# Optimization experiments

Hardware: AMD Instinct MI355X
Metric: run time of the kernel (lower is better)

The kernel has to match this reference:

```python
import jax, jax.numpy as jnp
import numpy as np
import math

HEADS = 4
DK = 64            # dim // heads
TEMP = 1.0
LMAX = 2048        # max segment length (for padded ragged attention)


def setup_inputs() -> dict:
    key = jax.random.key(0)
    ks = jax.random.split(key, 6)
    T, H, B = 1024, 256, 16
    # ragged lengths alternating 2048/1024 -> N = 24576
    lengths = np.tile(np.array([2048, 1024], dtype=np.int64), B // 2)
    N = int(lengths.sum())
    s = 1.0 / math.sqrt(H)
    return {
        "go_mat": jax.random.normal(ks[0], (T, H), jnp.float32),
        "node_h": jax.random.normal(ks[1], (N, H), jnp.float32),
        "Wq": jax.random.normal(ks[2], (H, H), jnp.float32) * s,
        "Wk": jax.random.normal(ks[3], (H, H), jnp.float32) * s,
        "Wv": jax.random.normal(ks[4], (H, H), jnp.float32) * s,
        "Wproj": jax.random.normal(ks[5], (H, H), jnp.float32) * s,
        "num_nodes_per_graph": jnp.asarray(lengths),
    }


def reference(go_mat, node_h, Wq, Wk, Wv, Wproj, num_nodes_per_graph):
    lengths = num_nodes_per_graph
    B = lengths.shape[0]
    N, H = node_h.shape
    T = go_mat.shape[0]

    # segment bookkeeping: graph id and within-graph offset for each node
    cum = jnp.cumsum(lengths)                       # [B]
    starts = cum - lengths                          # [B]
    g = jnp.searchsorted(cum, jnp.arange(N), side="right")  # [N] graph id
    off = jnp.arange(N) - starts[g]                 # [N] position within graph

    # projections (torch Linear: x @ W.T)
    Q = (go_mat @ Wq.T).reshape(T, HEADS, DK).transpose(1, 0, 2)   # [h,T,dk]
    K = node_h @ Wk.T                                              # [N,H]
    V = node_h @ Wv.T

    # scatter packed nodes into padded [B, Lmax, H]
    Kp = jnp.zeros((B, LMAX, H), K.dtype).at[g, off].set(K)
    Vp = jnp.zeros((B, LMAX, H), V.dtype).at[g, off].set(V)
    Kp = Kp.reshape(B, LMAX, HEADS, DK).transpose(0, 2, 1, 3)      # [B,h,L,dk]
    Vp = Vp.reshape(B, LMAX, HEADS, DK).transpose(0, 2, 1, 3)

    scores = jnp.einsum("htd,bhld->bhtl", Q, Kp) / (math.sqrt(DK) * TEMP)
    valid = jnp.arange(LMAX)[None, :] < lengths[:, None]           # [B,L]
    scores = jnp.where(valid[:, None, None, :], scores, jnp.float32(-1e30))
    attn = jax.nn.softmax(scores, axis=-1)                         # [B,h,T,L]

    ctx = jnp.einsum("bhtl,bhld->bhtd", attn, Vp)                  # [B,h,T,dk]
    ctx = ctx.transpose(0, 2, 1, 3).reshape(B, T, H)               # [B,T,H]
    return ctx @ Wproj.T
```

## Files before the change

### kernel.cpp

```cpp
#include <hip/hip_runtime.h>
#include <math.h>

#define HEADS 4
#define DK 64
#define HD 256

typedef __attribute__((ext_vector_type(8))) __bf16 bf16x8;
typedef __attribute__((ext_vector_type(4))) float floatx4;

union BF8 { ushort u[8]; bf16x8 v; };

__device__ __forceinline__ ushort f2bf(float f) {
  union { float f; unsigned u; } x; x.f = f;
  return (ushort)((x.u + 0x7FFF + ((x.u >> 16) & 1)) >> 16);
}
__device__ __forceinline__ ushort f2bf_fast(float f) {
  union { float f; unsigned u; } x; x.f = f;
  return (ushort)((x.u + 0x8000u) >> 16);
}

#define GLDS(g, l) __builtin_amdgcn_global_load_lds(                      \
    (const __attribute__((address_space(1))) unsigned*)(g),               \
    (__attribute__((address_space(3))) unsigned*)(l), 16, 0, 0)

__global__ __launch_bounds__(256) void cvt_swz(const float* __restrict__ x,
                                               ushort* __restrict__ y, int rows) {
  const int idx = blockIdx.x * 256 + threadIdx.x;
  const int row = idx >> 5, gr = idx & 31;
  if (row >= rows) return;
  const int chunk = gr >> 3, g = gr & 7;
  const float* src = x + (size_t)row * 256 + gr * 8;
  float4 a = *(const float4*)src;
  float4 bq = *(const float4*)(src + 4);
  const int phys = g ^ (row & 7);
  ushort* dst = y + (size_t)row * 256 + chunk * 64 + phys * 8;
  ushort4 o0 = {f2bf(a.x), f2bf(a.y), f2bf(a.z), f2bf(a.w)};
  ushort4 o1 = {f2bf(bq.x), f2bf(bq.y), f2bf(bq.z), f2bf(bq.w)};
  *(ushort4*)dst = o0;
  *(ushort4*)(dst + 4) = o1;
}

__global__ __launch_bounds__(256) void cvt_swz_w(const float* __restrict__ w0,
                                                 const float* __restrict__ w1,
                                                 const float* __restrict__ w2,
                                                 const float* __restrict__ w3,
                                                 ushort* __restrict__ y) {
  const float* srcs[4] = {w0, w1, w2, w3};
  const float* x = srcs[blockIdx.y];
  ushort* yo = y + (size_t)blockIdx.y * HD * HD;
  const int idx = blockIdx.x * 256 + threadIdx.x;
  const int row = idx >> 5, gr = idx & 31;
  const int chunk = gr >> 3, g = gr & 7;
  const float* src = x + (size_t)row * 256 + gr * 8;
  float4 a = *(const float4*)src;
  float4 bq = *(const float4*)(src + 4);
  const int phys = g ^ (row & 7);
  ushort* dst = yo + (size_t)row * 256 + chunk * 64 + phys * 8;
  ushort4 o0 = {f2bf(a.x), f2bf(a.y), f2bf(a.z), f2bf(a.w)};
  ushort4 o1 = {f2bf(bq.x), f2bf(bq.y), f2bf(bq.z), f2bf(bq.w)};
  *(ushort4*)dst = o0;
  *(ushort4*)(dst + 4) = o1;
}

template <int MODE>
__global__ __launch_bounds__(256) void gemm_bf16(const ushort* __restrict__ A,
                                                 const ushort* __restrict__ W,
                                                 ushort* __restrict__ C, int M,
                                                 int ldc) {
  __shared__ ushort As[128 * 64];
  __shared__ ushort Ws[64 * 64];
  const int tid = threadIdx.x, lane = tid & 63, w = tid >> 6;
  const int quad = lane >> 4, l15 = lane & 15;
  const int m0 = blockIdx.x * 128, n0 = blockIdx.y * 64;
  const int wm = w & 1, wn = w >> 1;

  floatx4 acc[4][2];
#pragma unroll
  for (int mt = 0; mt < 4; ++mt)
#pragma unroll
    for (int nt = 0; nt < 2; ++nt) acc[mt][nt] = (floatx4){0.f, 0.f, 0.f, 0.f};

  for (int k0 = 0; k0 < 256; k0 += 64) {
    __syncthreads();
#pragma unroll
    for (int t = 0; t < 4; ++t)
      GLDS(A + (size_t)(m0 + w * 32 + t * 8 + (lane >> 3)) * 256 + k0 + (lane & 7) * 8,
           &As[(w * 32 + t * 8) * 64]);
#pragma unroll
    for (int t = 0; t < 2; ++t)
      GLDS(W + (size_t)(n0 + w * 16 + t * 8 + (lane >> 3)) * 256 + k0 + (lane & 7) * 8,
           &Ws[(w * 16 + t * 8) * 64]);
    __syncthreads();

    bf16x8 af[4][2], bfr[2][2];
#pragma unroll
    for (int kk = 0; kk < 2; ++kk) {
      const int pg = ((kk * 4 + quad) ^ (l15 & 7)) * 8;
#pragma unroll
      for (int mt = 0; mt < 4; ++mt)
        af[mt][kk] = *(const bf16x8*)&As[(wm * 64 + mt * 16 + l15) * 64 + pg];
#pragma unroll
      for (int nt = 0; nt < 2; ++nt)
        bfr[nt][kk] = *(const bf16x8*)&Ws[(wn * 32 + nt * 16 + l15) * 64 + pg];
    }
#pragma unroll
    for (int kk = 0; kk < 2; ++kk)
#pragma unroll
      for (int mt = 0; mt < 4; ++mt)
#pragma unroll
        for (int nt = 0; nt < 2; ++nt)
          acc[mt][nt] = __builtin_amdgcn_mfma_f32_16x16x32_bf16(
              af[mt][kk], bfr[nt][kk], acc[mt][nt], 0, 0, 0);
  }

#pragma unroll
  for (int mt = 0; mt < 4; ++mt)
#pragma unroll
    for (int nt = 0; nt < 2; ++nt) {
      const int col = n0 + wn * 32 + nt * 16 + l15;
      if (MODE == 2) {
        const int d = col & 63;
        const int g = mt * 2 + (quad >> 1);
        const int node = m0 + wm * 64 + (g ^ (d & 7)) * 8 + (quad & 1) * 4;
        ushort4 o = {f2bf(acc[mt][nt][0]), f2bf(acc[mt][nt][1]),
                     f2bf(acc[mt][nt][2]), f2bf(acc[mt][nt][3])};
        *(ushort4*)&C[(size_t)col * ldc + node] = o;
      } else {
#pragma unroll
        for (int r = 0; r < 4; ++r) {
          const int row = m0 + wm * 64 + mt * 16 + quad * 4 + r;
          if (MODE == 3) {
            ((float*)C)[(size_t)row * 256 + col] = acc[mt][nt][r];
          } else {
            int cc = col;
            if (MODE == 1)
              cc = (col & ~63) | (((((col >> 3) & 7) ^ (row & 7))) << 3) | (col & 7);
            C[(size_t)row * 256 + cc] = f2bf(acc[mt][nt][r]);
          }
        }
      }
    }
}

__global__ __launch_bounds__(512, 4) void attn_mfma(
    const ushort* __restrict__ Qb, const ushort* __restrict__ Kg,
    const ushort* __restrict__ Vt, const int* __restrict__ lens,
    ushort* __restrict__ ctxb, int T, int N) {
  __shared__ ushort Ks[2][64 * 64];
  __shared__ ushort Vs[2][64 * 64];
  __shared__ ushort Ps[8 * 16 * 72];

  const int tid = threadIdx.x, lane = tid & 63, wave = tid >> 6;
  const int quad = lane >> 4, l15 = lane & 15;
  const int h = blockIdx.y, b = blockIdx.z;
  int start = 0;
  for (int i = 0; i < b; ++i) start += lens[i];
  const int len = lens[b];

  const int srow = wave * 8 + (lane >> 3);
  const int scol = (lane & 7) * 8;

  const int tq = blockIdx.x * 128 + wave * 16 + l15;
  bf16x8 qa[2];
#pragma unroll
  for (int kk = 0; kk < 2; ++kk)
    qa[kk] = *(const bf16x8*)(Qb + (size_t)tq * 256 + h * 64 + kk * 32 + quad * 8);

  BF8 onesu;
#pragma unroll
  for (int j = 0; j < 8; ++j) onesu.u[j] = 0x3F80;
  const bf16x8 ones = onesu.v;

  floatx4 o[4], lacc = (floatx4){0.f, 0.f, 0.f, 0.f};
#pragma unroll
  for (int n = 0; n < 4; ++n) o[n] = (floatx4){0.f, 0.f, 0.f, 0.f};

  const float sc = 0.18033688011112042f;
  ushort* pw = &Ps[wave * 16 * 72];

  GLDS(Kg + (size_t)(start + srow) * 256 + h * 64 + scol, &Ks[0][wave * 8 * 64]);
  GLDS(Vt + (size_t)(h * 64 + srow) * (size_t)N + start + scol, &Vs[0][wave * 8 * 64]);

  int buf = 0;
  for (int j0 = 0; j0 < len; j0 += 64, buf ^= 1) {
    __syncthreads();
    const int jn = j0 + 64;
    if (jn < len) {
      GLDS(Kg + (size_t)(start + jn + srow) * 256 + h * 64 + scol,
           &Ks[buf ^ 1][wave * 8 * 64]);
      GLDS(Vt + (size_t)(h * 64 + srow) * (size_t)N + start + jn + scol,
           &Vs[buf ^ 1][wave * 8 * 64]);
    }

    floatx4 st[4];
#pragma unroll
    for (int t = 0; t < 4; ++t) st[t] = (floatx4){0.f, 0.f, 0.f, 0.f};
#pragma unroll
    for (int kk = 0; kk < 2; ++kk) {
#pragma unroll
      for (int t = 0; t < 4; ++t) {
        bf16x8 kf = *(const bf16x8*)&Ks[buf][(t * 16 + l15) * 64 +
                                            ((kk * 4 + quad) ^ (l15 & 7)) * 8];
        st[t] = __builtin_amdgcn_mfma_f32_16x16x32_bf16(qa[kk], kf, st[t], 0, 0, 0);
      }
    }

    const bool full = jn <= len;
#pragma unroll
    for (int t = 0; t < 4; ++t) {
      const bool v = full || (j0 + t * 16 + l15 < len);
#pragma unroll
      for (int r = 0; r < 4; ++r) {
        const float u = v ? fmaf(st[t][r], sc, -32.0f) : -1e30f;
        pw[(quad * 4 + r) * 72 + t * 16 + l15] = f2bf_fast(exp2f(u));
      }
    }

#pragma unroll
    for (int ks = 0; ks < 2; ++ks) {
      bf16x8 pa = *(const bf16x8*)&pw[l15 * 72 + ks * 32 + quad * 8];
      lacc = __builtin_amdgcn_mfma_f32_16x16x32_bf16(pa, ones, lacc, 0, 0, 0);
#pragma unroll
      for (int n = 0; n < 4; ++n) {
        bf16x8 vf = *(const bf16x8*)&Vs[buf][(n * 16 + l15) * 64 +
                                            ((ks * 4 + quad) ^ (l15 & 7)) * 8];
        o[n] = __builtin_amdgcn_mfma_f32_16x16x32_bf16(pa, vf, o[n], 0, 0, 0);
      }
    }
  }

  float inv[4];
#pragma unroll
  for (int r = 0; r < 4; ++r) inv[r] = 1.0f / lacc[r];
  const int q0 = blockIdx.x * 128 + wave * 16 + quad * 4;
  ushort* cb = ctxb + ((size_t)b * T + q0) * 256;
#pragma unroll
  for (int n = 0; n < 4; ++n)
#pragma unroll
    for (int r = 0; r < 4; ++r) {
      const int colg = n * 2 + (l15 >> 3);
      const int cc = h * 64 + ((colg ^ ((q0 + r) & 7)) << 3) | (l15 & 7);
      cb[(size_t)r * 256 + cc] = f2bf(o[n][r] * inv[r]);
    }
}

extern "C" void kernel_launch(void* const* d_in, const int* in_sizes, int n_in,
                              void* d_out, int out_size, void* d_ws, size_t ws_size,
                              hipStream_t stream) {
  const float* go     = (const float*)d_in[0];
  const float* node_h = (const float*)d_in[1];
  const float* Wq     = (const float*)d_in[2];
  const float* Wk     = (const float*)d_in[3];
  const float* Wv     = (const float*)d_in[4];
  const float* Wproj  = (const float*)d_in[5];
  const int*   lens   = (const int*)d_in[6];

  const int T = in_sizes[0] / HD;
  const int N = in_sizes[1] / HD;
  const int B = in_sizes[6];

  char* p = (char*)d_ws;
  ushort* ctxb = (ushort*)p;            p += (size_t)B * T * HD * 2;
  ushort* nodebf = (ushort*)p;          p += (size_t)N * HD * 2;
  ushort* Kgb = (ushort*)p;             p += (size_t)N * HD * 2;
  ushort* Vtb = (ushort*)p;             p += (size_t)N * HD * 2;
  ushort* gobf = (ushort*)p;            p += (size_t)T * HD * 2;
  ushort* Qbf = (ushort*)p;             p += (size_t)T * HD * 2;
  ushort* wbf = (ushort*)p;             p += (size_t)4 * HD * HD * 2;
  ushort* wqbf = wbf;
  ushort* wkbf = wbf + (size_t)HD * HD;
  ushort* wvbf = wbf + (size_t)2 * HD * HD;
  ushort* wpbf = wbf + (size_t)3 * HD * HD;

  cvt_swz<<<(T * 32 + 255) / 256, 256, 0, stream>>>(go, gobf, T);
  cvt_swz<<<(N * 32 + 255) / 256, 256, 0, stream>>>(node_h, nodebf, N);
  cvt_swz_w<<<dim3(32, 4), 256, 0, stream>>>(Wq, Wk, Wv, Wproj, wbf);

  gemm_bf16<0><<<dim3(T / 128, 4), 256, 0, stream>>>(gobf, wqbf, Qbf, T, 0);
  gemm_bf16<1><<<dim3(N / 128, 4), 256, 0, stream>>>(nodebf, wkbf, Kgb, N, 0);
  gemm_bf16<2><<<dim3(N / 128, 4), 256, 0, stream>>>(nodebf, wvbf, Vtb, N, N);

  attn_mfma<<<dim3(T / 128, HEADS, B), 512, 0, stream>>>(Qbf, Kgb, Vtb, lens, ctxb, T, N);

  gemm_bf16<3><<<dim3((B * T) / 128, 4), 256, 0, stream>>>(ctxb, wpbf, (ushort*)d_out, B * T, 0);
}
```

Measured before the change: 185.8 us.

## Give each attention wave two query tiles and merge K/V projection kernels

The attention kernel drops to 256 threads per block, with each wave handling 32 queries (two 16-row tiles). Each K and V fragment read from LDS is therefore reused across two MFMAs, which halves LDS fragment traffic per FLOP. The row-sum is now accumulated in registers from the fp32 probabilities instead of through an MFMA against a ones vector, and scores are computed transposed so the P tile can be written as packed ushort4 stores. Separately, the K and V projections are merged into one launch, and V's transpose is staged through LDS for coalesced 16-byte stores. The costs are higher register pressure and fewer waves per block to hide latency.

```diff
diff --git a/kernel.cpp b/kernel.cpp
--- a/kernel.cpp
+++ b/kernel.cpp
@@ -7,8 +7,6 @@
 
 typedef __attribute__((ext_vector_type(8))) __bf16 bf16x8;
 typedef __attribute__((ext_vector_type(4))) float floatx4;
-
-union BF8 { ushort u[8]; bf16x8 v; };
 
 __device__ __forceinline__ ushort f2bf(float f) {
   union { float f; unsigned u; } x; x.f = f;
@@ -62,93 +60,125 @@
   *(ushort4*)(dst + 4) = o1;
 }
 
+#define GEMM_BODY(APTR, WPTR)                                                  \
+  floatx4 acc[4][2];                                                           \
+  _Pragma("unroll") for (int mt = 0; mt < 4; ++mt)                             \
+      _Pragma("unroll") for (int nt = 0; nt < 2; ++nt)                         \
+          acc[mt][nt] = (floatx4){0.f, 0.f, 0.f, 0.f};                         \
+  for (int k0 = 0; k0 < 256; k0 += 64) {                                       \
+    __syncthreads();                                                           \
+    _Pragma("unroll") for (int t = 0; t < 4; ++t)                              \
+        GLDS(APTR + (size_t)(m0 + w * 32 + t * 8 + (lane >> 3)) * 256 + k0 +   \
+                 (lane & 7) * 8,                                               \
+             &As[(w * 32 + t * 8) * 64]);                                      \
+    _Pragma("unroll") for (int t = 0; t < 2; ++t)                              \
+        GLDS(WPTR + (size_t)(n0 + w * 16 + t * 8 + (lane >> 3)) * 256 + k0 +   \
+                 (lane & 7) * 8,                                               \
+             &Ws[(w * 16 + t * 8) * 64]);                                      \
+    __syncthreads();                                                           \
+    bf16x8 af[4][2], bfr[2][2];                                                \
+    _Pragma("unroll") for (int kk = 0; kk < 2; ++kk) {                         \
+      const int pg = ((kk * 4 + quad) ^ (l15 & 7)) * 8;                        \
+      _Pragma("unroll") for (int mt = 0; mt < 4; ++mt)                         \
+          af[mt][kk] = *(const bf16x8*)&As[(wm * 64 + mt * 16 + l15) * 64 + pg]; \
+      _Pragma("unroll") for (int nt = 0; nt < 2; ++nt)                         \
+          bfr[nt][kk] = *(const bf16x8*)&Ws[(wn * 32 + nt * 16 + l15) * 64 + pg]; \
+    }                                                                          \
+    _Pragma("unroll") for (int kk = 0; kk < 2; ++kk)                           \
+        _Pragma("unroll") for (int mt = 0; mt < 4; ++mt)                       \
+            _Pragma("unroll") for (int nt = 0; nt < 2; ++nt)                   \
+                acc[mt][nt] = __builtin_amdgcn_mfma_f32_16x16x32_bf16(         \
+                    af[mt][kk], bfr[nt][kk], acc[mt][nt], 0, 0, 0);            \
+  }
+
 template <int MODE>
 __global__ __launch_bounds__(256) void gemm_bf16(const ushort* __restrict__ A,
                                                  const ushort* __restrict__ W,
-                                                 ushort* __restrict__ C, int M,
-                                                 int ldc) {
+                                                 ushort* __restrict__ C, int M) {
   __shared__ ushort As[128 * 64];
   __shared__ ushort Ws[64 * 64];
   const int tid = threadIdx.x, lane = tid & 63, w = tid >> 6;
   const int quad = lane >> 4, l15 = lane & 15;
   const int m0 = blockIdx.x * 128, n0 = blockIdx.y * 64;
   const int wm = w & 1, wn = w >> 1;
-
-  floatx4 acc[4][2];
-#pragma unroll
-  for (int mt = 0; mt < 4; ++mt)
-#pragma unroll
-    for (int nt = 0; nt < 2; ++nt) acc[mt][nt] = (floatx4){0.f, 0.f, 0.f, 0.f};
-
-  for (int k0 = 0; k0 < 256; k0 += 64) {
-    __syncthreads();
-#pragma unroll
-    for (int t = 0; t < 4; ++t)
-      GLDS(A + (size_t)(m0 + w * 32 + t * 8 + (lane >> 3)) * 256 + k0 + (lane & 7) * 8,
-           &As[(w * 32 + t * 8) * 64]);
-#pragma unroll
-    for (int t = 0; t < 2; ++t)
-      GLDS(W + (size_t)(n0 + w * 16 + t * 8 + (lane >> 3)) * 256 + k0 + (lane & 7) * 8,
-           &Ws[(w * 16 + t * 8) * 64]);
-    __syncthreads();
-
-    bf16x8 af[4][2], bfr[2][2];
-#pragma unroll
-    for (int kk = 0; kk < 2; ++kk) {
-      const int pg = ((kk * 4 + quad) ^ (l15 & 7)) * 8;
-#pragma unroll
-      for (int mt = 0; mt < 4; ++mt)
-        af[mt][kk] = *(const bf16x8*)&As[(wm * 64 + mt * 16 + l15) * 64 + pg];
-#pragma unroll
-      for (int nt = 0; nt < 2; ++nt)
-        bfr[nt][kk] = *(const bf16x8*)&Ws[(wn * 32 + nt * 16 + l15) * 64 + pg];
-    }
-#pragma unroll
-    for (int kk = 0; kk < 2; ++kk)
-#pragma unroll
-      for (int mt = 0; mt < 4; ++mt)
-#pragma unroll
-        for (int nt = 0; nt < 2; ++nt)
-          acc[mt][nt] = __builtin_amdgcn_mfma_f32_16x16x32_bf16(
-              af[mt][kk], bfr[nt][kk], acc[mt][nt], 0, 0, 0);
-  }
-
+  GEMM_BODY(A, W)
 #pragma unroll
   for (int mt = 0; mt < 4; ++mt)
 #pragma unroll
     for (int nt = 0; nt < 2; ++nt) {
       const int col = n0 + wn * 32 + nt * 16 + l15;
-      if (MODE == 2) {
-        const int d = col & 63;
-        const int g = mt * 2 + (quad >> 1);
-        const int node = m0 + wm * 64 + (g ^ (d & 7)) * 8 + (quad & 1) * 4;
+#pragma unroll
+      for (int r = 0; r < 4; ++r) {
+        const int row = m0 + wm * 64 + mt * 16 + quad * 4 + r;
+        if (MODE == 3)
+          ((float*)C)[(size_t)row * 256 + col] = acc[mt][nt][r];
+        else
+          C[(size_t)row * 256 + col] = f2bf(acc[mt][nt][r]);
+      }
+    }
+}
+
+__global__ __launch_bounds__(256) void gemm_kv(const ushort* __restrict__ A,
+                                               const ushort* __restrict__ Wk,
+                                               const ushort* __restrict__ Wv,
+                                               ushort* __restrict__ Ck,
+                                               ushort* __restrict__ Cv, int N) {
+  __shared__ ushort As[128 * 64];
+  __shared__ ushort Ws[64 * 64];
+  __shared__ ushort Ts[64 * 136];
+  const int tid = threadIdx.x, lane = tid & 63, w = tid >> 6;
+  const int quad = lane >> 4, l15 = lane & 15;
+  const int m0 = blockIdx.x * 128, n0 = blockIdx.y * 64;
+  const int wm = w & 1, wn = w >> 1;
+  const ushort* W = blockIdx.z ? Wv : Wk;
+  GEMM_BODY(A, W)
+  if (blockIdx.z == 0) {
+#pragma unroll
+    for (int mt = 0; mt < 4; ++mt)
+#pragma unroll
+      for (int nt = 0; nt < 2; ++nt) {
+        const int col = n0 + wn * 32 + nt * 16 + l15;
+#pragma unroll
+        for (int r = 0; r < 4; ++r) {
+          const int row = m0 + wm * 64 + mt * 16 + quad * 4 + r;
+          const int cc =
+              (col & ~63) | (((((col >> 3) & 7) ^ (row & 7))) << 3) | (col & 7);
+          Ck[(size_t)row * 256 + cc] = f2bf(acc[mt][nt][r]);
+        }
+      }
+  } else {
+#pragma unroll
+    for (int mt = 0; mt < 4; ++mt)
+#pragma unroll
+      for (int nt = 0; nt < 2; ++nt) {
+        const int d_rel = wn * 32 + nt * 16 + l15;
+        const int node_rel = wm * 64 + mt * 16 + quad * 4;
         ushort4 o = {f2bf(acc[mt][nt][0]), f2bf(acc[mt][nt][1]),
                      f2bf(acc[mt][nt][2]), f2bf(acc[mt][nt][3])};
-        *(ushort4*)&C[(size_t)col * ldc + node] = o;
-      } else {
-#pragma unroll
-        for (int r = 0; r < 4; ++r) {
-          const int row = m0 + wm * 64 + mt * 16 + quad * 4 + r;
-          if (MODE == 3) {
-            ((float*)C)[(size_t)row * 256 + col] = acc[mt][nt][r];
-          } else {
-            int cc = col;
-            if (MODE == 1)
-              cc = (col & ~63) | (((((col >> 3) & 7) ^ (row & 7))) << 3) | (col & 7);
-            C[(size_t)row * 256 + cc] = f2bf(acc[mt][nt][r]);
-          }
-        }
-      }
-    }
-}
-
-__global__ __launch_bounds__(512, 4) void attn_mfma(
+        *(ushort4*)&Ts[d_rel * 136 + node_rel] = o;
+      }
+    __syncthreads();
+    const int d_rel = tid >> 2;
+    const int cseg = (tid & 3) * 32;
+    const int d = n0 + d_rel;
+#pragma unroll
+    for (int i = 0; i < 4; ++i) {
+      const int col = cseg + i * 8;
+      const int gl = (col >> 3) & 7;
+      const int chunk = col >> 6;
+      uint4 v = *(const uint4*)&Ts[d_rel * 136 + col];
+      *(uint4*)&Cv[(size_t)d * N + m0 + chunk * 64 + ((gl ^ (d & 7)) << 3)] = v;
+    }
+  }
+}
+
+__global__ __launch_bounds__(256, 3) void attn_mfma(
     const ushort* __restrict__ Qb, const ushort* __restrict__ Kg,
     const ushort* __restrict__ Vt, const int* __restrict__ lens,
     ushort* __restrict__ ctxb, int T, int N) {
   __shared__ ushort Ks[2][64 * 64];
   __shared__ ushort Vs[2][64 * 64];
-  __shared__ ushort Ps[8 * 16 * 72];
+  __shared__ ushort Ps[4 * 32 * 72];
 
   const int tid = threadIdx.x, lane = tid & 63, wave = tid >> 6;
   const int quad = lane >> 4, l15 = lane & 15;
@@ -157,91 +187,132 @@
   for (int i = 0; i < b; ++i) start += lens[i];
   const int len = lens[b];
 
-  const int srow = wave * 8 + (lane >> 3);
+  const int q0 = blockIdx.x * 128 + wave * 32;
+  bf16x8 qb[2][2];
+#pragma unroll
+  for (int qt = 0; qt < 2; ++qt)
+#pragma unroll
+    for (int kk = 0; kk < 2; ++kk)
+      qb[qt][kk] = *(const bf16x8*)(Qb + (size_t)(q0 + qt * 16 + l15) * 256 +
+                                    h * 64 + kk * 32 + quad * 8);
+
+  floatx4 o[2][4];
+#pragma unroll
+  for (int qt = 0; qt < 2; ++qt)
+#pragma unroll
+    for (int nt = 0; nt < 4; ++nt) o[qt][nt] = (floatx4){0.f, 0.f, 0.f, 0.f};
+  float lsum[2] = {0.f, 0.f};
+
+  const float sc = 0.18033688011112042f;
+  ushort* pw = &Ps[wave * 32 * 72];
+
+  const int srow = (lane >> 3);
   const int scol = (lane & 7) * 8;
 
-  const int tq = blockIdx.x * 128 + wave * 16 + l15;
-  bf16x8 qa[2];
-#pragma unroll
-  for (int kk = 0; kk < 2; ++kk)
-    qa[kk] = *(const bf16x8*)(Qb + (size_t)tq * 256 + h * 64 + kk * 32 + quad * 8);
-
-  BF8 onesu;
-#pragma unroll
-  for (int j = 0; j < 8; ++j) onesu.u[j] = 0x3F80;
-  const bf16x8 ones = onesu.v;
-
-  floatx4 o[4], lacc = (floatx4){0.f, 0.f, 0.f, 0.f};
-#pragma unroll
-  for (int n = 0; n < 4; ++n) o[n] = (floatx4){0.f, 0.f, 0.f, 0.f};
-
-  const float sc = 0.18033688011112042f;
-  ushort* pw = &Ps[wave * 16 * 72];
-
-  GLDS(Kg + (size_t)(start + srow) * 256 + h * 64 + scol, &Ks[0][wave * 8 * 64]);
-  GLDS(Vt + (size_t)(h * 64 + srow) * (size_t)N + start + scol, &Vs[0][wave * 8 * 64]);
+  GLDS(Kg + (size_t)(start + wave * 8 + srow) * 256 + h * 64 + scol,
+       &Ks[0][(wave * 8) * 64]);
+  GLDS(Kg + (size_t)(start + wave * 8 + 32 + srow) * 256 + h * 64 + scol,
+       &Ks[0][(wave * 8 + 32) * 64]);
+  GLDS(Vt + (size_t)(h * 64 + wave * 8 + srow) * (size_t)N + start + scol,
+       &Vs[0][(wave * 8) * 64]);
+  GLDS(Vt + (size_t)(h * 64 + wave * 8 + 32 + srow) * (size_t)N + start + scol,
+       &Vs[0][(wave * 8 + 32) * 64]);
 
   int buf = 0;
   for (int j0 = 0; j0 < len; j0 += 64, buf ^= 1) {
     __syncthreads();
     const int jn = j0 + 64;
     if (jn < len) {
-      GLDS(Kg + (size_t)(start + jn + srow) * 256 + h * 64 + scol,
-           &Ks[buf ^ 1][wave * 8 * 64]);
-      GLDS(Vt + (size_t)(h * 64 + srow) * (size_t)N + start + jn + scol,
-           &Vs[buf ^ 1][wave * 8 * 64]);
-    }
-
-    floatx4 st[4];
-#pragma unroll
-    for (int t = 0; t < 4; ++t) st[t] = (floatx4){0.f, 0.f, 0.f, 0.f};
+      GLDS(Kg + (size_t)(start + jn + wave * 8 + srow) * 256 + h * 64 + scol,
+           &Ks[buf ^ 1][(wave * 8) * 64]);
+      GLDS(Kg + (size_t)(start + jn + wave * 8 + 32 + srow) * 256 + h * 64 + scol,
+           &Ks[buf ^ 1][(wave * 8 + 32) * 64]);
+      GLDS(Vt + (size_t)(h * 64 + wave * 8 + srow) * (size_t)N + start + jn + scol,
+           &Vs[buf ^ 1][(wave * 8) * 64]);
+      GLDS(Vt + (size_t)(h * 64 + wave * 8 + 32 + srow) * (size_t)N + start + jn + scol,
+           &Vs[buf ^ 1][(wave * 8 + 32) * 64]);
+    }
+
+    floatx4 st[4][2];
+#pragma unroll
+    for (int t = 0; t < 4; ++t)
+#pragma unroll
+      for (int qt = 0; qt < 2; ++qt) st[t][qt] = (floatx4){0.f, 0.f, 0.f, 0.f};
 #pragma unroll
     for (int kk = 0; kk < 2; ++kk) {
 #pragma unroll
       for (int t = 0; t < 4; ++t) {
         bf16x8 kf = *(const bf16x8*)&Ks[buf][(t * 16 + l15) * 64 +
                                             ((kk * 4 + quad) ^ (l15 & 7)) * 8];
-        st[t] = __builtin_amdgcn_mfma_f32_16x16x32_bf16(qa[kk], kf, st[t], 0, 0, 0);
-      }
-    }
-
-    const bool full = jn <= len;
-#pragma unroll
-    for (int t = 0; t < 4; ++t) {
-      const bool v = full || (j0 + t * 16 + l15 < len);
+        st[t][0] = __builtin_amdgcn_mfma_f32_16x16x32_bf16(kf, qb[0][kk], st[t][0], 0, 0, 0);
+        st[t][1] = __builtin_amdgcn_mfma_f32_16x16x32_bf16(kf, qb[1][kk], st[t][1], 0, 0, 0);
+      }
+    }
+
+    if (jn <= len) {
+#pragma unroll
+      for (int t = 0; t < 4; ++t)
+#pragma unroll
+        for (int qt = 0; qt < 2; ++qt) {
+          float p[4];
+#pragma unroll
+          for (int r = 0; r < 4; ++r) p[r] = exp2f(fmaf(st[t][qt][r], sc, -32.0f));
+          lsum[qt] += (p[0] + p[1]) + (p[2] + p[3]);
+          ushort4 pk = {f2bf_fast(p[0]), f2bf_fast(p[1]), f2bf_fast(p[2]),
+                        f2bf_fast(p[3])};
+          *(ushort4*)&pw[(qt * 16 + l15) * 72 + t * 16 + quad * 4] = pk;
+        }
+    } else {
+#pragma unroll
+      for (int t = 0; t < 4; ++t)
+#pragma unroll
+        for (int qt = 0; qt < 2; ++qt) {
+          float p[4];
+#pragma unroll
+          for (int r = 0; r < 4; ++r) {
+            const bool v = (j0 + t * 16 + quad * 4 + r) < len;
+            p[r] = v ? exp2f(fmaf(st[t][qt][r], sc, -32.0f)) : 0.0f;
+          }
+          lsum[qt] += (p[0] + p[1]) + (p[2] + p[3]);
+          ushort4 pk = {f2bf_fast(p[0]), f2bf_fast(p[1]), f2bf_fast(p[2]),
+                        f2bf_fast(p[3])};
+          *(ushort4*)&pw[(qt * 16 + l15) * 72 + t * 16 + quad * 4] = pk;
+        }
+    }
+
+#pragma unroll
+    for (int ks = 0; ks < 2; ++ks) {
+      bf16x8 pa0 = *(const bf16x8*)&pw[l15 * 72 + ks * 32 + quad * 8];
+      bf16x8 pa1 = *(const bf16x8*)&pw[(16 + l15) * 72 + ks * 32 + quad * 8];
+#pragma unroll
+      for (int nt = 0; nt < 4; ++nt) {
+        bf16x8 vf = *(const bf16x8*)&Vs[buf][(nt * 16 + l15) * 64 +
+                                            ((ks * 4 + quad) ^ (l15 & 7)) * 8];
+        o[0][nt] = __builtin_amdgcn_mfma_f32_16x16x32_bf16(pa0, vf, o[0][nt], 0, 0, 0);
+        o[1][nt] = __builtin_amdgcn_mfma_f32_16x16x32_bf16(pa1, vf, o[1][nt], 0, 0, 0);
+      }
+    }
+  }
+
+#pragma unroll
+  for (int qt = 0; qt < 2; ++qt) {
+    float lt = lsum[qt];
+    lt += __shfl_xor(lt, 16);
+    lt += __shfl_xor(lt, 32);
+    float inv[4];
+#pragma unroll
+    for (int r = 0; r < 4; ++r) inv[r] = 1.0f / __shfl(lt, quad * 4 + r);
+    const int qrow0 = q0 + qt * 16 + quad * 4;
+    ushort* cb = ctxb + ((size_t)b * T + qrow0) * 256;
+#pragma unroll
+    for (int nt = 0; nt < 4; ++nt)
 #pragma unroll
       for (int r = 0; r < 4; ++r) {
-        const float u = v ? fmaf(st[t][r], sc, -32.0f) : -1e30f;
-        pw[(quad * 4 + r) * 72 + t * 16 + l15] = f2bf_fast(exp2f(u));
-      }
-    }
-
-#pragma unroll
-    for (int ks = 0; ks < 2; ++ks) {
-      bf16x8 pa = *(const bf16x8*)&pw[l15 * 72 + ks * 32 + quad * 8];
-      lacc = __builtin_amdgcn_mfma_f32_16x16x32_bf16(pa, ones, lacc, 0, 0, 0);
-#pragma unroll
-      for (int n = 0; n < 4; ++n) {
-        bf16x8 vf = *(const bf16x8*)&Vs[buf][(n * 16 + l15) * 64 +
-                                            ((ks * 4 + quad) ^ (l15 & 7)) * 8];
-        o[n] = __builtin_amdgcn_mfma_f32_16x16x32_bf16(pa, vf, o[n], 0, 0, 0);
-      }
-    }
+        const int colg = nt * 2 + (l15 >> 3);
+        const int cc = h * 64 + (((colg ^ ((qrow0 + r) & 7)) << 3) | (l15 & 7));
+        cb[(size_t)r * 256 + cc] = f2bf(o[qt][nt][r] * inv[r]);
+      }
   }
-
-  float inv[4];
-#pragma unroll
-  for (int r = 0; r < 4; ++r) inv[r] = 1.0f / lacc[r];
-  const int q0 = blockIdx.x * 128 + wave * 16 + quad * 4;
-  ushort* cb = ctxb + ((size_t)b * T + q0) * 256;
-#pragma unroll
-  for (int n = 0; n < 4; ++n)
-#pragma unroll
-    for (int r = 0; r < 4; ++r) {
-      const int colg = n * 2 + (l15 >> 3);
-      const int cc = h * 64 + ((colg ^ ((q0 + r) & 7)) << 3) | (l15 & 7);
-      cb[(size_t)r * 256 + cc] = f2bf(o[n][r] * inv[r]);
-    }
 }
 
 extern "C" void kernel_launch(void* const* d_in, const int* in_sizes, int n_in,
@@ -276,11 +347,10 @@
   cvt_swz<<<(N * 32 + 255) / 256, 256, 0, stream>>>(node_h, nodebf, N);
   cvt_swz_w<<<dim3(32, 4), 256, 0, stream>>>(Wq, Wk, Wv, Wproj, wbf);
 
-  gemm_bf16<0><<<dim3(T / 128, 4), 256, 0, stream>>>(gobf, wqbf, Qbf, T, 0);
-  gemm_bf16<1><<<dim3(N / 128, 4), 256, 0, stream>>>(nodebf, wkbf, Kgb, N, 0);
-  gemm_bf16<2><<<dim3(N / 128, 4), 256, 0, stream>>>(nodebf, wvbf, Vtb, N, N);
-
-  attn_mfma<<<dim3(T / 128, HEADS, B), 512, 0, stream>>>(Qbf, Kgb, Vtb, lens, ctxb, T, N);
-
-  gemm_bf16<3><<<dim3((B * T) / 128, 4), 256, 0, stream>>>(ctxb, wpbf, (ushort*)d_out, B * T, 0);
-}
+  gemm_bf16<0><<<dim3(T / 128, 4), 256, 0, stream>>>(gobf, wqbf, Qbf, T);
+  gemm_kv<<<dim3(N / 128, 4, 2), 256, 0, stream>>>(nodebf, wkbf, wvbf, Kgb, Vtb, N);
+
+  attn_mfma<<<dim3(T / 128, HEADS, B), 256, 0, stream>>>(Qbf, Kgb, Vtb, lens, ctxb, T, N);
+
+  gemm_bf16<3><<<dim3((B * T) / 128, 4), 256, 0, stream>>>(ctxb, wpbf, (ushort*)d_out, B * T);
+}
```

New measurement: 194.7 us. +4.8%, slower.

## Split attention over fixed 1024-key chunks and add combine pass

Applied to the files above, without the earlier changes.

Attention now splits each ragged segment into 1024-key chunks, one block per chunk, so long and short graphs give equal-sized work items and the grid is balanced. Each block handles 32 query rows per wave with a transposed score MFMA, sums row totals in registers instead of an extra ones-MFMA, and packs exp values with perm. A new combine kernel adds up the partial outputs and row sums and normalises them. This costs extra fp32 partial traffic through memory and one more launch. The two input conversions are also merged into one launch, and nodebf shares workspace with the partial buffers.

```diff
diff --git a/kernel.cpp b/kernel.cpp
--- a/kernel.cpp
+++ b/kernel.cpp
@@ -8,32 +8,44 @@
 typedef __attribute__((ext_vector_type(8))) __bf16 bf16x8;
 typedef __attribute__((ext_vector_type(4))) float floatx4;
 
-union BF8 { ushort u[8]; bf16x8 v; };
-
 __device__ __forceinline__ ushort f2bf(float f) {
   union { float f; unsigned u; } x; x.f = f;
   return (ushort)((x.u + 0x7FFF + ((x.u >> 16) & 1)) >> 16);
 }
-__device__ __forceinline__ ushort f2bf_fast(float f) {
-  union { float f; unsigned u; } x; x.f = f;
-  return (ushort)((x.u + 0x8000u) >> 16);
+
+#if __has_builtin(__builtin_amdgcn_exp2f)
+#define EXP2(x) __builtin_amdgcn_exp2f(x)
+#else
+#define EXP2(x) exp2f(x)
+#endif
+
+__device__ __forceinline__ unsigned pack_bf2(float lo, float hi) {
+  union { float f; unsigned u; } a, b;
+  a.f = lo; b.f = hi;
+  return __builtin_amdgcn_perm(b.u + 0x8000u, a.u + 0x8000u, 0x07060302u);
 }
 
 #define GLDS(g, l) __builtin_amdgcn_global_load_lds(                      \
     (const __attribute__((address_space(1))) unsigned*)(g),               \
     (__attribute__((address_space(3))) unsigned*)(l), 16, 0, 0)
 
-__global__ __launch_bounds__(256) void cvt_swz(const float* __restrict__ x,
-                                               ushort* __restrict__ y, int rows) {
+__global__ __launch_bounds__(256) void cvt_all(const float* __restrict__ go,
+                                               const float* __restrict__ nh,
+                                               ushort* __restrict__ gobf,
+                                               ushort* __restrict__ nodebf,
+                                               int T, int N) {
   const int idx = blockIdx.x * 256 + threadIdx.x;
   const int row = idx >> 5, gr = idx & 31;
-  if (row >= rows) return;
+  if (row >= T + N) return;
+  const float* x; ushort* y; int r;
+  if (row < T) { x = go; y = gobf; r = row; }
+  else         { x = nh; y = nodebf; r = row - T; }
   const int chunk = gr >> 3, g = gr & 7;
-  const float* src = x + (size_t)row * 256 + gr * 8;
+  const float* src = x + (size_t)r * 256 + gr * 8;
   float4 a = *(const float4*)src;
   float4 bq = *(const float4*)(src + 4);
-  const int phys = g ^ (row & 7);
-  ushort* dst = y + (size_t)row * 256 + chunk * 64 + phys * 8;
+  const int phys = g ^ (r & 7);
+  ushort* dst = y + (size_t)r * 256 + chunk * 64 + phys * 8;
   ushort4 o0 = {f2bf(a.x), f2bf(a.y), f2bf(a.z), f2bf(a.w)};
   ushort4 o1 = {f2bf(bq.x), f2bf(bq.y), f2bf(bq.z), f2bf(bq.w)};
   *(ushort4*)dst = o0;
@@ -67,8 +79,8 @@
                                                  const ushort* __restrict__ W,
                                                  ushort* __restrict__ C, int M,
                                                  int ldc) {
-  __shared__ ushort As[128 * 64];
-  __shared__ ushort Ws[64 * 64];
+  __shared__ __align__(16) ushort As[128 * 64];
+  __shared__ __align__(16) ushort Ws[64 * 64];
   const int tid = threadIdx.x, lane = tid & 63, w = tid >> 6;
   const int quad = lane >> 4, l15 = lane & 15;
   const int m0 = blockIdx.x * 128, n0 = blockIdx.y * 64;
@@ -142,106 +154,192 @@
     }
 }
 
-__global__ __launch_bounds__(512, 4) void attn_mfma(
+__global__ __launch_bounds__(256, 3) void attn_split(
     const ushort* __restrict__ Qb, const ushort* __restrict__ Kg,
     const ushort* __restrict__ Vt, const int* __restrict__ lens,
-    ushort* __restrict__ ctxb, int T, int N) {
-  __shared__ ushort Ks[2][64 * 64];
-  __shared__ ushort Vs[2][64 * 64];
-  __shared__ ushort Ps[8 * 16 * 72];
+    float* __restrict__ Opart, float* __restrict__ Lpart,
+    int T, int N, int Bc) {
+  __shared__ __align__(16) ushort Ks[2][64 * 64];
+  __shared__ __align__(16) ushort Vs[2][64 * 64];
+  __shared__ __align__(16) ushort Ps[4 * 32 * 72];
 
   const int tid = threadIdx.x, lane = tid & 63, wave = tid >> 6;
   const int quad = lane >> 4, l15 = lane & 15;
-  const int h = blockIdx.y, b = blockIdx.z;
-  int start = 0;
-  for (int i = 0; i < b; ++i) start += lens[i];
-  const int len = lens[b];
-
-  const int srow = wave * 8 + (lane >> 3);
+  const int h = blockIdx.y;
+
+  int z = blockIdx.z, b, start = 0, len = 0, off = -1;
+  for (b = 0; b < Bc; ++b) {
+    len = lens[b];
+    const int s = (len + 1023) >> 10;
+    if (z < s) { off = z << 10; break; }
+    z -= s; start += len;
+  }
+  if (off < 0) return;
+  const int kcnt = min(1024, len - off);
+  const int kbeg = start + off;
+
+  const int q0 = blockIdx.x * 128 + wave * 32;
+  bf16x8 qb[2][2];
+#pragma unroll
+  for (int qt = 0; qt < 2; ++qt)
+#pragma unroll
+    for (int kk = 0; kk < 2; ++kk)
+      qb[qt][kk] = *(const bf16x8*)(Qb + (size_t)(q0 + qt * 16 + l15) * 256 +
+                                    h * 64 + kk * 32 + quad * 8);
+
+  floatx4 o[2][4];
+#pragma unroll
+  for (int qt = 0; qt < 2; ++qt)
+#pragma unroll
+    for (int nt = 0; nt < 4; ++nt) o[qt][nt] = (floatx4){0.f, 0.f, 0.f, 0.f};
+  float lsum[2] = {0.f, 0.f};
+
+  const float sc = 0.18033688011112042f;
+  ushort* pw = &Ps[wave * 32 * 72];
+
+  const int srow = lane >> 3;
   const int scol = (lane & 7) * 8;
 
-  const int tq = blockIdx.x * 128 + wave * 16 + l15;
-  bf16x8 qa[2];
-#pragma unroll
-  for (int kk = 0; kk < 2; ++kk)
-    qa[kk] = *(const bf16x8*)(Qb + (size_t)tq * 256 + h * 64 + kk * 32 + quad * 8);
-
-  BF8 onesu;
-#pragma unroll
-  for (int j = 0; j < 8; ++j) onesu.u[j] = 0x3F80;
-  const bf16x8 ones = onesu.v;
-
-  floatx4 o[4], lacc = (floatx4){0.f, 0.f, 0.f, 0.f};
-#pragma unroll
-  for (int n = 0; n < 4; ++n) o[n] = (floatx4){0.f, 0.f, 0.f, 0.f};
-
-  const float sc = 0.18033688011112042f;
-  ushort* pw = &Ps[wave * 16 * 72];
-
-  GLDS(Kg + (size_t)(start + srow) * 256 + h * 64 + scol, &Ks[0][wave * 8 * 64]);
-  GLDS(Vt + (size_t)(h * 64 + srow) * (size_t)N + start + scol, &Vs[0][wave * 8 * 64]);
+  GLDS(Kg + (size_t)(kbeg + wave * 8 + srow) * 256 + h * 64 + scol,
+       &Ks[0][(wave * 8) * 64]);
+  GLDS(Kg + (size_t)(kbeg + wave * 8 + 32 + srow) * 256 + h * 64 + scol,
+       &Ks[0][(wave * 8 + 32) * 64]);
+  GLDS(Vt + (size_t)(h * 64 + wave * 8 + srow) * (size_t)N + kbeg + scol,
+       &Vs[0][(wave * 8) * 64]);
+  GLDS(Vt + (size_t)(h * 64 + wave * 8 + 32 + srow) * (size_t)N + kbeg + scol,
+       &Vs[0][(wave * 8 + 32) * 64]);
 
   int buf = 0;
-  for (int j0 = 0; j0 < len; j0 += 64, buf ^= 1) {
+  for (int j0 = 0; j0 < kcnt; j0 += 64, buf ^= 1) {
     __syncthreads();
     const int jn = j0 + 64;
-    if (jn < len) {
-      GLDS(Kg + (size_t)(start + jn + srow) * 256 + h * 64 + scol,
-           &Ks[buf ^ 1][wave * 8 * 64]);
-      GLDS(Vt + (size_t)(h * 64 + srow) * (size_t)N + start + jn + scol,
-           &Vs[buf ^ 1][wave * 8 * 64]);
-    }
-
-    floatx4 st[4];
-#pragma unroll
-    for (int t = 0; t < 4; ++t) st[t] = (floatx4){0.f, 0.f, 0.f, 0.f};
+    if (jn < kcnt) {
+      GLDS(Kg + (size_t)(kbeg + jn + wave * 8 + srow) * 256 + h * 64 + scol,
+           &Ks[buf ^ 1][(wave * 8) * 64]);
+      GLDS(Kg + (size_t)(kbeg + jn + wave * 8 + 32 + srow) * 256 + h * 64 + scol,
+           &Ks[buf ^ 1][(wave * 8 + 32) * 64]);
+      GLDS(Vt + (size_t)(h * 64 + wave * 8 + srow) * (size_t)N + kbeg + jn + scol,
+           &Vs[buf ^ 1][(wave * 8) * 64]);
+      GLDS(Vt + (size_t)(h * 64 + wave * 8 + 32 + srow) * (size_t)N + kbeg + jn + scol,
+           &Vs[buf ^ 1][(wave * 8 + 32) * 64]);
+    }
+
+    floatx4 st[4][2];
+#pragma unroll
+    for (int t = 0; t < 4; ++t)
+#pragma unroll
+      for (int qt = 0; qt < 2; ++qt) st[t][qt] = (floatx4){0.f, 0.f, 0.f, 0.f};
 #pragma unroll
     for (int kk = 0; kk < 2; ++kk) {
 #pragma unroll
       for (int t = 0; t < 4; ++t) {
         bf16x8 kf = *(const bf16x8*)&Ks[buf][(t * 16 + l15) * 64 +
                                             ((kk * 4 + quad) ^ (l15 & 7)) * 8];
-        st[t] = __builtin_amdgcn_mfma_f32_16x16x32_bf16(qa[kk], kf, st[t], 0, 0, 0);
+        st[t][0] = __builtin_amdgcn_mfma_f32_16x16x32_bf16(kf, qb[0][kk], st[t][0], 0, 0, 0);
+        st[t][1] = __builtin_amdgcn_mfma_f32_16x16x32_bf16(kf, qb[1][kk], st[t][1], 0, 0, 0);
       }
     }
 
-    const bool full = jn <= len;
-#pragma unroll
-    for (int t = 0; t < 4; ++t) {
-      const bool v = full || (j0 + t * 16 + l15 < len);
-#pragma unroll
-      for (int r = 0; r < 4; ++r) {
-        const float u = v ? fmaf(st[t][r], sc, -32.0f) : -1e30f;
-        pw[(quad * 4 + r) * 72 + t * 16 + l15] = f2bf_fast(exp2f(u));
+    if (jn <= kcnt) {
+#pragma unroll
+      for (int t = 0; t < 4; ++t)
+#pragma unroll
+        for (int qt = 0; qt < 2; ++qt) {
+          float p[4];
+#pragma unroll
+          for (int r = 0; r < 4; ++r) p[r] = EXP2(fmaf(st[t][qt][r], sc, -32.0f));
+          lsum[qt] += (p[0] + p[1]) + (p[2] + p[3]);
+          uint2 pk = {pack_bf2(p[0], p[1]), pack_bf2(p[2], p[3])};
+          *(uint2*)&pw[(qt * 16 + l15) * 72 + t * 16 + quad * 4] = pk;
+        }
+    } else {
+#pragma unroll
+      for (int t = 0; t < 4; ++t)
+#pragma unroll
+        for (int qt = 0; qt < 2; ++qt) {
+          float p[4];
+#pragma unroll
+          for (int r = 0; r < 4; ++r) {
+            const bool v = (j0 + t * 16 + quad * 4 + r) < kcnt;
+            p[r] = v ? EXP2(fmaf(st[t][qt][r], sc, -32.0f)) : 0.0f;
+          }
+          lsum[qt] += (p[0] + p[1]) + (p[2] + p[3]);
+          uint2 pk = {pack_bf2(p[0], p[1]), pack_bf2(p[2], p[3])};
+          *(uint2*)&pw[(qt * 16 + l15) * 72 + t * 16 + quad * 4] = pk;
+        }
+    }
+
+#pragma unroll
+    for (int ks = 0; ks < 2; ++ks) {
+      bf16x8 pa0 = *(const bf16x8*)&pw[l15 * 72 + ks * 32 + quad * 8];
+      bf16x8 pa1 = *(const bf16x8*)&pw[(16 + l15) * 72 + ks * 32 + quad * 8];
+#pragma unroll
+      for (int nt = 0; nt < 4; ++nt) {
+        bf16x8 vf = *(const bf16x8*)&Vs[buf][(nt * 16 + l15) * 64 +
+                                            ((ks * 4 + quad) ^ (l15 & 7)) * 8];
+        o[0][nt] = __builtin_amdgcn_mfma_f32_16x16x32_bf16(pa0, vf, o[0][nt], 0, 0, 0);
+        o[1][nt] = __builtin_amdgcn_mfma_f32_16x16x32_bf16(pa1, vf, o[1][nt], 0, 0, 0);
       }
     }
-
-#pragma unroll
-    for (int ks = 0; ks < 2; ++ks) {
-      bf16x8 pa = *(const bf16x8*)&pw[l15 * 72 + ks * 32 + quad * 8];
-      lacc = __builtin_amdgcn_mfma_f32_16x16x32_bf16(pa, ones, lacc, 0, 0, 0);
-#pragma unroll
-      for (int n = 0; n < 4; ++n) {
-        bf16x8 vf = *(const bf16x8*)&Vs[buf][(n * 16 + l15) * 64 +
-                                            ((ks * 4 + quad) ^ (l15 & 7)) * 8];
-        o[n] = __builtin_amdgcn_mfma_f32_16x16x32_bf16(pa, vf, o[n], 0, 0, 0);
-      }
-    }
-  }
-
-  float inv[4];
-#pragma unroll
-  for (int r = 0; r < 4; ++r) inv[r] = 1.0f / lacc[r];
-  const int q0 = blockIdx.x * 128 + wave * 16 + quad * 4;
-  ushort* cb = ctxb + ((size_t)b * T + q0) * 256;
-#pragma unroll
-  for (int n = 0; n < 4; ++n)
-#pragma unroll
-    for (int r = 0; r < 4; ++r) {
-      const int colg = n * 2 + (l15 >> 3);
-      const int cc = h * 64 + ((colg ^ ((q0 + r) & 7)) << 3) | (l15 & 7);
-      cb[(size_t)r * 256 + cc] = f2bf(o[n][r] * inv[r]);
-    }
+  }
+
+  const int part = (blockIdx.z * HEADS + h) * (T >> 7) + blockIdx.x;
+  float* op = Opart + (size_t)part * (128 * 64);
+#pragma unroll
+  for (int qt = 0; qt < 2; ++qt) {
+#pragma unroll
+    for (int nt = 0; nt < 4; ++nt)
+#pragma unroll
+      for (int r = 0; r < 4; ++r)
+        op[(wave * 32 + qt * 16 + quad * 4 + r) * 64 + nt * 16 + l15] = o[qt][nt][r];
+    float lt = lsum[qt];
+    lt += __shfl_xor(lt, 16);
+    lt += __shfl_xor(lt, 32);
+    if (lane < 16)
+      Lpart[(size_t)part * 128 + wave * 32 + qt * 16 + lane] = lt;
+  }
+}
+
+__global__ __launch_bounds__(256) void combine(const float* __restrict__ Opart,
+                                               const float* __restrict__ Lpart,
+                                               const int* __restrict__ lens,
+                                               ushort* __restrict__ ctxb, int T) {
+  const int t = threadIdx.x;
+  const int row = blockIdx.x * 64 + (t >> 2);
+  const int h = t & 3;
+  const int b = row / T;
+  const int tq = row - b * T;
+  const int qx = tq >> 7, qr = tq & 127;
+  const int QX = T >> 7;
+  int z0 = 0;
+  for (int i = 0; i < b; ++i) z0 += (lens[i] + 1023) >> 10;
+  const int ns = (lens[b] + 1023) >> 10;
+
+  float l = 0.f;
+  float4 acc[16];
+#pragma unroll
+  for (int g = 0; g < 16; ++g) acc[g] = make_float4(0.f, 0.f, 0.f, 0.f);
+  for (int s = 0; s < ns; ++s) {
+    const size_t part = (size_t)((z0 + s) * HEADS + h) * QX + qx;
+    l += Lpart[part * 128 + qr];
+    const float4* src = (const float4*)(Opart + part * 8192 + (size_t)qr * 64);
+#pragma unroll
+    for (int g = 0; g < 16; ++g) {
+      float4 v = src[g];
+      acc[g].x += v.x; acc[g].y += v.y; acc[g].z += v.z; acc[g].w += v.w;
+    }
+  }
+  const float inv = 1.0f / l;
+  ushort* dst = ctxb + (size_t)row * 256 + h * 64;
+#pragma unroll
+  for (int gg = 0; gg < 8; ++gg) {
+    const float4 a = acc[gg * 2], c = acc[gg * 2 + 1];
+    const int phys = gg ^ (row & 7);
+    ushort4 o0 = {f2bf(a.x * inv), f2bf(a.y * inv), f2bf(a.z * inv), f2bf(a.w * inv)};
+    ushort4 o1 = {f2bf(c.x * inv), f2bf(c.y * inv), f2bf(c.z * inv), f2bf(c.w * inv)};
+    *(ushort4*)&dst[phys * 8] = o0;
+    *(ushort4*)&dst[phys * 8 + 4] = o1;
+  }
 }
 
 extern "C" void kernel_launch(void* const* d_in, const int* in_sizes, int n_in,
@@ -258,29 +356,34 @@
   const int T = in_sizes[0] / HD;
   const int N = in_sizes[1] / HD;
   const int B = in_sizes[6];
+  const int NSPL = N >> 10;
+  const int QX = T / 128;
 
   char* p = (char*)d_ws;
-  ushort* ctxb = (ushort*)p;            p += (size_t)B * T * HD * 2;
-  ushort* nodebf = (ushort*)p;          p += (size_t)N * HD * 2;
-  ushort* Kgb = (ushort*)p;             p += (size_t)N * HD * 2;
-  ushort* Vtb = (ushort*)p;             p += (size_t)N * HD * 2;
-  ushort* gobf = (ushort*)p;            p += (size_t)T * HD * 2;
-  ushort* Qbf = (ushort*)p;             p += (size_t)T * HD * 2;
-  ushort* wbf = (ushort*)p;             p += (size_t)4 * HD * HD * 2;
+  ushort* Kgb  = (ushort*)p;  p += (size_t)N * HD * 2;
+  ushort* Vtb  = (ushort*)p;  p += (size_t)N * HD * 2;
+  ushort* Qbf  = (ushort*)p;  p += (size_t)T * HD * 2;
+  ushort* gobf = (ushort*)p;  p += (size_t)T * HD * 2;
+  ushort* ctxb = (ushort*)p;  p += (size_t)B * T * HD * 2;
+  ushort* wbf  = (ushort*)p;  p += (size_t)4 * HD * HD * 2;
   ushort* wqbf = wbf;
   ushort* wkbf = wbf + (size_t)HD * HD;
   ushort* wvbf = wbf + (size_t)2 * HD * HD;
   ushort* wpbf = wbf + (size_t)3 * HD * HD;
-
-  cvt_swz<<<(T * 32 + 255) / 256, 256, 0, stream>>>(go, gobf, T);
-  cvt_swz<<<(N * 32 + 255) / 256, 256, 0, stream>>>(node_h, nodebf, N);
+  ushort* nodebf = (ushort*)p;
+  float* Opart = (float*)p;   p += (size_t)NSPL * HEADS * QX * 8192 * 4;
+  float* Lpart = (float*)p;   p += (size_t)NSPL * HEADS * QX * 128 * 4;
+
+  cvt_all<<<((T + N) * 32 + 255) / 256, 256, 0, stream>>>(go, node_h, gobf, nodebf, T, N);
   cvt_swz_w<<<dim3(32, 4), 256, 0, stream>>>(Wq, Wk, Wv, Wproj, wbf);
 
   gemm_bf16<0><<<dim3(T / 128, 4), 256, 0, stream>>>(gobf, wqbf, Qbf, T, 0);
   gemm_bf16<1><<<dim3(N / 128, 4), 256, 0, stream>>>(nodebf, wkbf, Kgb, N, 0);
   gemm_bf16<2><<<dim3(N / 128, 4), 256, 0, stream>>>(nodebf, wvbf, Vtb, N, N);
 
-  attn_mfma<<<dim3(T / 128, HEADS, B), 512, 0, stream>>>(Qbf, Kgb, Vtb, lens, ctxb, T, N);
+  attn_split<<<dim3(QX, HEADS, NSPL), 256, 0, stream>>>(Qbf, Kgb, Vtb, lens,
+                                                        Opart, Lpart, T, N, B);
+  combine<<<(B * T) / 64, 256, 0, stream>>>(Opart, Lpart, lens, ctxb, T);
 
   gemm_bf16<3><<<dim3((B * T) / 128, 4), 256, 0, stream>>>(ctxb, wpbf, (ushort*)d_out, B * T, 0);
 }
```

After: 167.0 us. -10.1%, faster.
